# Kernel tuning notes

Hardware: AMD Instinct MI355X
Metric: run time of the kernel (lower is better)

The kernel has to match this reference:

```python
import jax, jax.numpy as jnp
import numpy as np

N, E, D, H, ED, L, G = 20000, 320000, 256, 256, 64, 4, 64


def setup_inputs() -> dict:
    key = jax.random.key(0)
    ks = jax.random.split(key, 24)
    w = lambda k, shape: jax.random.normal(k, shape, dtype=jnp.float32) * 0.05
    inp = {
        "x": jax.random.normal(ks[0], (N, D), dtype=jnp.float32),
        "edge_attr": jax.random.normal(ks[1], (E, ED), dtype=jnp.float32),
        "pos": jax.random.normal(ks[2], (N, 3), dtype=jnp.float32),
        "edge_index": jax.random.randint(ks[3], (2, E), 0, N, dtype=jnp.int32),
        "batch": jnp.sort(jax.random.randint(ks[4], (N,), 0, G, dtype=jnp.int32)),
        # stacked per-layer params [L, ...]
        "node_w": w(ks[5], (L, D, H)), "node_b": w(ks[6], (L, H)),
        "edge_w": w(ks[7], (L, ED, H)), "edge_b": w(ks[8], (L, H)),
        "msg_w1": w(ks[9], (L, 2 * H + 1, H)), "msg_b1": w(ks[10], (L, H)),
        "msg_w2": w(ks[11], (L, H, H)), "msg_b2": w(ks[12], (L, H)),
        "upd_w1": w(ks[13], (L, H, H)), "upd_b1": w(ks[14], (L, H)),
        "upd_w2": w(ks[15], (L, H, D)), "upd_b2": w(ks[16], (L, D)),
        # global pooling head
        "fc_w1": w(ks[17], (D, H)), "fc_b1": w(ks[18], (H,)),
        "fc_w2": w(ks[19], (H, 1)), "fc_b2": w(ks[20], (1,)),
    }
    return inp


def reference(x, edge_attr, pos, edge_index, batch,
              node_w, node_b, edge_w, edge_b,
              msg_w1, msg_b1, msg_w2, msg_b2,
              upd_w1, upd_b1, upd_w2, upd_b2,
              fc_w1, fc_b1, fc_w2, fc_b2):
    src = edge_index[0]  # x_j (source / message sender)
    dst = edge_index[1]  # x_i (target / aggregation index)
    # edge distance depends only on fixed pos/edge_index: compute once
    edge_dist = jnp.linalg.norm(pos[src] - pos[dst], axis=1, keepdims=True)  # [E,1]
    silu = jax.nn.silu
    for l in range(L):
        x_emb = x @ node_w[l] + node_b[l]                    # [N,H]
        e_emb = edge_attr @ edge_w[l] + edge_b[l]            # [E,H]
        m_in = jnp.concatenate([x_emb[dst], x_emb[src], edge_dist], axis=-1)  # [E,2H+1]
        m = silu(m_in @ msg_w1[l] + msg_b1[l])
        m = silu(m @ msg_w2[l] + msg_b2[l]) + e_emb          # [E,H]
        aggr = jax.ops.segment_sum(m, dst, num_segments=N)   # scatter-add into target nodes
        x = silu(aggr @ upd_w1[l] + upd_b1[l]) @ upd_w2[l] + upd_b2[l]  # [N,D]
    pooled = jax.ops.segment_sum(x, batch, num_segments=G)   # [G,D]
    out = silu(pooled @ fc_w1 + fc_b1) @ fc_w2 + fc_b2       # [G,1]
    return out
```

## Files before the change

kernel.cpp:

```cpp
#include <hip/hip_runtime.h>
#include <hip/hip_bf16.h>
#include <math.h>

#define N_NODES 20000
#define N_EDGES 320000
#define NGRAPH 64

typedef __attribute__((ext_vector_type(8))) short short8;
typedef __attribute__((ext_vector_type(4))) short short4x;
typedef __attribute__((ext_vector_type(4))) float f32x4;
typedef __attribute__((ext_vector_type(4))) unsigned uint4v;
typedef __attribute__((ext_vector_type(2))) unsigned uint2v;

__device__ __forceinline__ float silu_f(float v){ return v / (1.0f + __expf(-v)); }
__device__ __forceinline__ float bf2f(short s){
  unsigned u = ((unsigned)(unsigned short)s) << 16;
  float f; __builtin_memcpy(&f, &u, 4); return f;
}
__device__ __forceinline__ short f2bf(float f){
  unsigned u; __builtin_memcpy(&u, &f, 4);
  unsigned r = (u + 0x7FFFu + ((u >> 16) & 1u)) >> 16;
  return (short)r;
}
__device__ __forceinline__ unsigned pkcvt(float lo, float hi){
  unsigned r;
  asm("v_cvt_pk_bf16_f32 %0, %1, %2" : "=v"(r) : "v"(lo), "v"(hi));
  return r;
}
__device__ __forceinline__ float bf_lo(unsigned w){
  unsigned u = w << 16; float f; __builtin_memcpy(&f, &u, 4); return f;
}
__device__ __forceinline__ float bf_hi(unsigned w){
  unsigned u = w & 0xFFFF0000u; float f; __builtin_memcpy(&f, &u, 4); return f;
}

__global__ void k_hist(const int* __restrict__ ei, int* __restrict__ cnt){
  int e = blockIdx.x*256 + threadIdx.x;
  if (e >= N_EDGES) return;
  atomicAdd(&cnt[ei[N_EDGES + e]], 1);
}

__global__ void k_scan(const int* __restrict__ cnt, int* __restrict__ row_ptr,
                       int* __restrict__ off){
  __shared__ int ssum[256];
  int t = threadIdx.x;
  const int CHK = (N_NODES + 255)/256;
  int base = t*CHK;
  int s = 0;
  for(int i=0;i<CHK;i++){ int idx=base+i; if(idx<N_NODES) s += cnt[idx]; }
  ssum[t]=s; __syncthreads();
  for(int o=1;o<256;o<<=1){
    int v = (t>=o)? ssum[t-o] : 0;
    __syncthreads();
    ssum[t] += v;
    __syncthreads();
  }
  int pre = (t==0)? 0 : ssum[t-1];
  for(int i=0;i<CHK;i++){
    int idx=base+i; if(idx>=N_NODES) break;
    row_ptr[idx]=pre; off[idx]=pre; pre += cnt[idx];
  }
  if(t==255) row_ptr[N_NODES]=pre;
}

__global__ void k_scatter(const int* __restrict__ ei, int* __restrict__ off,
                          int* __restrict__ src_s, int* __restrict__ dst_s,
                          int* __restrict__ eid_s){
  int e = blockIdx.x*256 + threadIdx.x;
  if (e >= N_EDGES) return;
  int d = ei[N_EDGES + e];
  int p = atomicAdd(&off[d], 1);
  dst_s[p]=d; src_s[p]=ei[e]; eid_s[p]=e;
}

__global__ void k_dist_s(const int* __restrict__ src_s, const int* __restrict__ dst_s,
                         const float* __restrict__ pos, float* __restrict__ dist_s){
  int i = blockIdx.x*256 + threadIdx.x;
  if (i >= N_EDGES) return;
  int s = src_s[i], d = dst_s[i];
  float dx = pos[s*3+0]-pos[d*3+0];
  float dy = pos[s*3+1]-pos[d*3+1];
  float dz = pos[s*3+2]-pos[d*3+2];
  dist_s[i] = sqrtf(dx*dx+dy*dy+dz*dz);
}

__global__ void k_eaagg_s(const int* __restrict__ row_ptr, const int* __restrict__ eid_s,
                          const float* __restrict__ edge_attr, float* __restrict__ EA){
  int sub = threadIdx.x>>6, j = threadIdx.x&63;
  int d = blockIdx.x*4 + sub;
  if (d >= N_NODES) return;
  int b = row_ptr[d], e = row_ptr[d+1];
  float s = 0.f;
  for(int i=b;i<e;i++) s += edge_attr[(size_t)eid_s[i]*64 + j];
  EA[(size_t)d*96 + j] = s;
  if (j < 32) EA[(size_t)d*96 + 64 + j] = (j==0) ? (float)(e-b) : 0.f;
}

__global__ void k_f2b(const float* __restrict__ S, short* __restrict__ D, int n4){
  int i = blockIdx.x*256 + threadIdx.x;
  if (i >= n4) return;
  float4 v = ((const float4*)S)[i];
  uint2v o;
  o[0] = pkcvt(v.x, v.y);
  o[1] = pkcvt(v.z, v.w);
  *(uint2v*)&D[i*4] = o;
}

__global__ void k_transW(const float* __restrict__ msg_w1, const float* __restrict__ msg_w2,
                         const float* __restrict__ upd_w1, const float* __restrict__ upd_w2,
                         short* __restrict__ wT){
  int z = blockIdx.z; int l = z/5, w = z%5;
  const float* S;
  switch(w){
    case 0: S = msg_w1 + (size_t)l*513*256; break;
    case 1: S = msg_w1 + (size_t)l*513*256 + 256*256; break;
    case 2: S = msg_w2 + (size_t)l*256*256; break;
    case 3: S = upd_w1 + (size_t)l*256*256; break;
    default: S = upd_w2 + (size_t)l*256*256; break;
  }
  short* D = wT + (size_t)z*65536;
  __shared__ float t[32][33];
  int bx = blockIdx.x*32, by = blockIdx.y*32;
  int lx = threadIdx.x & 31, ly = threadIdx.x >> 5;
  #pragma unroll
  for(int r=0;r<4;r++){ int k = ly + r*8; t[k][lx] = S[(size_t)(by+k)*256 + bx+lx]; }
  __syncthreads();
  #pragma unroll
  for(int r=0;r<4;r++){
    int n = ly + r*8;
    D[(size_t)(bx+n)*256 + by+lx] = f2bf(t[lx][n]);
  }
}

__global__ void k_uw1ext(const short* __restrict__ wT, const float* __restrict__ edge_w,
                         const float* __restrict__ edge_b, short* __restrict__ uw1ext4){
  int n = blockIdx.x, l = blockIdx.y, tid = threadIdx.x;
  const short* uw1T = wT + (size_t)(l*5+3)*65536;
  short* dst = uw1ext4 + (size_t)l*256*352 + (size_t)n*352;
  dst[tid] = uw1T[(size_t)n*256 + tid];
  if (tid < 96){
    int c = tid;
    float s = 0.f;
    if (c < 64){
      const float* er = edge_w + (size_t)l*64*256 + (size_t)c*256;
      for(int m=0;m<256;m++) s += bf2f(uw1T[(size_t)n*256+m])*er[m];
    } else if (c == 64){
      const float* er = edge_b + (size_t)l*256;
      for(int m=0;m<256;m++) s += bf2f(uw1T[(size_t)n*256+m])*er[m];
    }
    dst[256 + c] = f2bf(s);
  }
}

__global__ void k_biasm_acc(const float* __restrict__ node_b, const float* __restrict__ msg_w1,
                            const float* __restrict__ msg_b1, float* __restrict__ biasm4){
  int j = threadIdx.x;
  int b = blockIdx.x, l = blockIdx.y;
  const float* nb  = node_b + l*256;
  const float* w1  = msg_w1 + (size_t)l*513*256;
  float* biasm = biasm4 + l*256;
  if (b == 16){ atomicAdd(&biasm[j], msg_b1[l*256+j]); return; }
  float s = 0.f;
  for(int k = b*16; k < b*16+16; k++)
    s += nb[k]*(w1[(size_t)k*256+j] + w1[(size_t)(256+k)*256+j]);
  atomicAdd(&biasm[j], s);
}

__global__ void k_biasfold(const float* __restrict__ upd_b2, const short* __restrict__ WabT4,
                           float* __restrict__ biasm4){
  int l = blockIdx.x + 1;
  int j = threadIdx.x;
  const float* ub2 = upd_b2 + (size_t)(l-1)*256;
  const short* W = WabT4 + (size_t)l*131072;
  float s = 0.f;
  for(int k=0;k<256;k++)
    s += ub2[k]*(bf2f(W[(size_t)j*256+k]) + bf2f(W[(size_t)(256+j)*256+k]));
  biasm4[l*256 + j] += s;
}

template<int K_REAL, int K_LDS, int OBF16>
__global__ __launch_bounds__(256)
void k_gemm_mfma(const short* __restrict__ A, const short* __restrict__ BT,
                 short* __restrict__ Cb, int M, int Nld,
                 int AzStr, int BzStr, int CzStr){
  __shared__ __align__(16) short As[32][K_LDS];
  const int CHL = K_LDS/8, CH = K_REAL/8;
  int tid = threadIdx.x;
  int zz = blockIdx.z;
  const short* Ab = A + (size_t)zz*AzStr;
  BT += (size_t)zz*BzStr;
  int m0 = blockIdx.y*32, n0 = blockIdx.x*256;
  for(int c = tid; c < 32*CHL; c += 256){
    int row = c / CHL, ch = c % CHL;
    uint4v v = (uint4v){0u,0u,0u,0u};
    if (ch < CH) v = *(const uint4v*)&Ab[(size_t)(m0+row)*K_REAL + ch*8];
    *(uint4v*)&As[row][(ch ^ (row&7))*8] = v;
  }
  __syncthreads();
  int wid = tid>>6, lane = tid&63, l15 = lane&15, lq = lane>>4;
  int ncol0 = n0 + wid*64;
  f32x4 acc[2][4];
  #pragma unroll
  for(int mt=0;mt<2;mt++)
    #pragma unroll
    for(int nt=0;nt<4;nt++) acc[mt][nt] = (f32x4){0.f,0.f,0.f,0.f};
  for(int k0=0;k0<K_REAL;k0+=32){
    int kc = k0 + 8*lq;
    short8 a[2], b[4];
    #pragma unroll
    for(int mt=0;mt<2;mt++){
      int row = mt*16 + l15;
      a[mt] = *(const short8*)&As[row][kc ^ ((row&7)<<3)];
    }
    #pragma unroll
    for(int nt=0;nt<4;nt++){
      int col = ncol0 + nt*16 + l15;
      b[nt] = *(const short8*)&BT[(size_t)col*K_REAL + kc];
    }
    #pragma unroll
    for(int mt=0;mt<2;mt++)
      #pragma unroll
      for(int nt=0;nt<4;nt++)
        acc[mt][nt] = __builtin_amdgcn_mfma_f32_16x16x32_bf16(a[mt], b[nt], acc[mt][nt], 0, 0, 0);
  }
  #pragma unroll
  for(int mt=0;mt<2;mt++){
    #pragma unroll
    for(int nt=0;nt<4;nt++){
      int col = ncol0 + nt*16 + l15;
      unsigned w01 = pkcvt(acc[mt][nt][0], acc[mt][nt][1]);
      unsigned w23 = pkcvt(acc[mt][nt][2], acc[mt][nt][3]);
      size_t base = (size_t)zz*CzStr + (size_t)(m0 + mt*16 + lq*4)*Nld + col;
      Cb[base]          = (short)(w01 & 0xFFFF);
      Cb[base +   Nld]  = (short)(w01>>16);
      Cb[base + 2*Nld]  = (short)(w23 & 0xFFFF);
      Cb[base + 3*Nld]  = (short)(w23>>16);
    }
  }
}

template<int K_REAL, int K_LDS, int AF32, int AEXT, int BIAS, int ACT, int OF32, int OBF16>
__global__ __launch_bounds__(256)
void k_gemm64(const void* __restrict__ A, const float* __restrict__ A2,
              const short* __restrict__ BT,
              const float* __restrict__ bias, float* __restrict__ Cf,
              short* __restrict__ Cb, int M, int Nld){
  __shared__ __align__(16) short As[64][K_LDS];
  const int CHL = K_LDS/8, CH = K_REAL/8;
  int tid = threadIdx.x;
  const short* Ab = (const short*)A;
  const float* Af = (const float*)A;
  int m0 = blockIdx.y*64, n0 = blockIdx.x*256;
  for(int c = tid; c < 64*CHL; c += 256){
    int row = c / CHL, ch = c % CHL;
    uint4v v = (uint4v){0u,0u,0u,0u};
    int grow = m0 + row;
    if (grow < M){
      if (AEXT){
        if (ch < 32){
          float4 f0 = *(const float4*)&Af[(size_t)grow*256 + ch*8];
          float4 f1 = *(const float4*)&Af[(size_t)grow*256 + ch*8 + 4];
          v[0]=pkcvt(f0.x,f0.y); v[1]=pkcvt(f0.z,f0.w); v[2]=pkcvt(f1.x,f1.y); v[3]=pkcvt(f1.z,f1.w);
        } else if (ch < 44){
          float4 f0 = *(const float4*)&A2[(size_t)grow*96 + (ch-32)*8];
          float4 f1 = *(const float4*)&A2[(size_t)grow*96 + (ch-32)*8 + 4];
          v[0]=pkcvt(f0.x,f0.y); v[1]=pkcvt(f0.z,f0.w); v[2]=pkcvt(f1.x,f1.y); v[3]=pkcvt(f1.z,f1.w);
        }
      } else if (ch < CH) {
        if (AF32){
          float4 f0 = *(const float4*)&Af[(size_t)grow*K_REAL + ch*8];
          float4 f1 = *(const float4*)&Af[(size_t)grow*K_REAL + ch*8 + 4];
          v[0]=pkcvt(f0.x,f0.y); v[1]=pkcvt(f0.z,f0.w); v[2]=pkcvt(f1.x,f1.y); v[3]=pkcvt(f1.z,f1.w);
        } else {
          v = *(const uint4v*)&Ab[(size_t)grow*K_REAL + ch*8];
        }
      }
    }
    *(uint4v*)&As[row][(ch ^ (row&7))*8] = v;
  }
  __syncthreads();
  int wid = tid>>6, lane = tid&63, l15 = lane&15, lq = lane>>4;
  int ncol0 = n0 + wid*64;
  f32x4 acc[4][4];
  #pragma unroll
  for(int mt=0;mt<4;mt++)
    #pragma unroll
    for(int nt=0;nt<4;nt++) acc[mt][nt] = (f32x4){0.f,0.f,0.f,0.f};
  for(int k0=0;k0<K_REAL;k0+=32){
    int kc = k0 + 8*lq;
    short8 a[4], b[4];
    #pragma unroll
    for(int mt=0;mt<4;mt++){
      int row = mt*16 + l15;
      a[mt] = *(const short8*)&As[row][kc ^ ((row&7)<<3)];
    }
    #pragma unroll
    for(int nt=0;nt<4;nt++){
      int col = ncol0 + nt*16 + l15;
      b[nt] = *(const short8*)&BT[(size_t)col*K_REAL + kc];
    }
    #pragma unroll
    for(int mt=0;mt<4;mt++)
      #pragma unroll
      for(int nt=0;nt<4;nt++)
        acc[mt][nt] = __builtin_amdgcn_mfma_f32_16x16x32_bf16(a[mt], b[nt], acc[mt][nt], 0, 0, 0);
  }
  #pragma unroll
  for(int mt=0;mt<4;mt++){
    int row0 = m0 + mt*16 + lq*4;
    if (row0 >= M) continue;
    #pragma unroll
    for(int nt=0;nt<4;nt++){
      int col = ncol0 + nt*16 + l15;
      float bb = BIAS ? bias[col] : 0.f;
      float vv[4];
      #pragma unroll
      for(int r=0;r<4;r++){
        float v = acc[mt][nt][r] + bb;
        if (ACT) v = silu_f(v);
        vv[r] = v;
      }
      if (OF32){
        #pragma unroll
        for(int r=0;r<4;r++)
          if (row0 + r < M)
            Cf[(size_t)(row0+r)*Nld + col] = vv[r];
      }
      if (OBF16){
        unsigned w01 = pkcvt(vv[0], vv[1]);
        unsigned w23 = pkcvt(vv[2], vv[3]);
        short ss[4] = {(short)(w01&0xFFFF),(short)(w01>>16),(short)(w23&0xFFFF),(short)(w23>>16)};
        #pragma unroll
        for(int r=0;r<4;r++)
          if (row0 + r < M)
            Cb[(size_t)(row0+r)*Nld + col] = ss[r];
      }
    }
  }
}

__global__ __launch_bounds__(256)
void k_edge_mfma(const short* __restrict__ t_ab,
                 const float* __restrict__ dist_s,
                 const int* __restrict__ src_s, const int* __restrict__ dst_s,
                 const float* __restrict__ w1c, const float* __restrict__ biasm,
                 const short* __restrict__ w2T, const float* __restrict__ b2,
                 float* __restrict__ aggr)
{
  __shared__ __align__(16) unsigned char ulds[256*34*2];
  short (*h)[256] = (short(*)[256])ulds;
  short* outl = (short*)ulds;
  __shared__ int sdst[32], ssrc[32];
  __shared__ float sdist[32];
  int tid = threadIdx.x;
  int e0 = blockIdx.x*32;
  if (tid < 32){
    sdst[tid] = dst_s[e0 + tid];
    ssrc[tid] = src_s[e0 + tid];
    sdist[tid] = dist_s[e0 + tid];
  }
  __syncthreads();
  int wid = tid>>6, lane = tid&63;
  int half = lane>>5, cl = lane&31;
  float wc8[8], bm8[8];
  {
    float4 w0 = *(const float4*)&w1c[8*cl], w1v = *(const float4*)&w1c[8*cl+4];
    float4 b0 = *(const float4*)&biasm[8*cl], b1v = *(const float4*)&biasm[8*cl+4];
    wc8[0]=w0.x; wc8[1]=w0.y; wc8[2]=w0.z; wc8[3]=w0.w;
    wc8[4]=w1v.x; wc8[5]=w1v.y; wc8[6]=w1v.z; wc8[7]=w1v.w;
    bm8[0]=b0.x; bm8[1]=b0.y; bm8[2]=b0.z; bm8[3]=b0.w;
    bm8[4]=b1v.x; bm8[5]=b1v.y; bm8[6]=b1v.z; bm8[7]=b1v.w;
  }
  #pragma unroll
  for(int p=0;p<4;p++){
    int e = wid*8 + p*2 + half;
    int d = sdst[e], s = ssrc[e];
    float de = sdist[e];
    short8 va = *(const short8*)&t_ab[(size_t)d*512 + 8*cl];
    short8 vb = *(const short8*)&t_ab[(size_t)s*512 + 256 + 8*cl];
    float f[8];
    #pragma unroll
    for(int i=0;i<8;i++)
      f[i] = silu_f(bf2f(va[i]) + bf2f(vb[i]) + de*wc8[i] + bm8[i]);
    uint4v hv;
    hv[0]=pkcvt(f[0],f[1]); hv[1]=pkcvt(f[2],f[3]); hv[2]=pkcvt(f[4],f[5]); hv[3]=pkcvt(f[6],f[7]);
    *(uint4v*)&h[e][(8*cl) ^ ((e&7)<<3)] = hv;
  }
  __syncthreads();

  int l15 = lane & 15, lq = lane >> 4;
  int nb = wid*64;
  f32x4 acc[2][4];
  #pragma unroll
  for(int mt=0;mt<2;mt++)
    #pragma unroll
    for(int nt=0;nt<4;nt++) acc[mt][nt] = (f32x4){0.f,0.f,0.f,0.f};

  for(int k0=0;k0<256;k0+=32){
    int kc = k0 + 8*lq;
    short8 a[2], b[4];
    #pragma unroll
    for(int mt=0;mt<2;mt++){
      int row = mt*16 + l15;
      a[mt] = *(const short8*)&h[row][kc ^ ((row&7)<<3)];
    }
    #pragma unroll
    for(int nt=0;nt<4;nt++){
      int col = nb + nt*16 + l15;
      b[nt] = *(const short8*)&w2T[(size_t)col*256 + kc];
    }
    #pragma unroll
    for(int mt=0;mt<2;mt++)
      #pragma unroll
      for(int nt=0;nt<4;nt++)
        acc[mt][nt] = __builtin_amdgcn_mfma_f32_16x16x32_bf16(a[mt], b[nt], acc[mt][nt], 0, 0, 0);
  }
  __syncthreads();

  #pragma unroll
  for(int mt=0;mt<2;mt++){
    #pragma unroll
    for(int nt=0;nt<4;nt++){
      int col = nb + nt*16 + l15;
      float bb = b2[col];
      float s0 = silu_f(acc[mt][nt][0] + bb);
      float s1 = silu_f(acc[mt][nt][1] + bb);
      float s2 = silu_f(acc[mt][nt][2] + bb);
      float s3 = silu_f(acc[mt][nt][3] + bb);
      unsigned* d32 = (unsigned*)&outl[col*34 + mt*16 + lq*4];
      d32[0] = pkcvt(s0, s1);
      d32[1] = pkcvt(s2, s3);
    }
  }
  __syncthreads();

  int j = tid;
  float accu = 0.f;
  int prev = sdst[0];
  #pragma unroll
  for(int e2=0;e2<32;e2+=2){
    unsigned w = *(const unsigned*)&outl[j*34 + e2];
    int d0 = sdst[e2], d1 = sdst[e2+1];
    if (d0 != prev){
      atomicAdd(&aggr[(size_t)prev*256 + j], accu);
      accu = 0.f; prev = d0;
    }
    accu += bf_lo(w);
    if (d1 != prev){
      atomicAdd(&aggr[(size_t)prev*256 + j], accu);
      accu = 0.f; prev = d1;
    }
    accu += bf_hi(w);
  }
  atomicAdd(&aggr[(size_t)prev*256 + j], accu);
}

__global__ void k_ghist(const int* __restrict__ batch, int* __restrict__ gcnt){
  int n = blockIdx.x*256 + threadIdx.x;
  if (n >= N_NODES) return;
  atomicAdd(&gcnt[batch[n]], 1);
}
__global__ void k_gscan(const int* __restrict__ gcnt, int* __restrict__ gptr){
  if (threadIdx.x == 0){
    int s = 0;
    for(int g=0; g<NGRAPH; g++){ gptr[g]=s; s += gcnt[g]; }
    gptr[NGRAPH] = s;
  }
}
__global__ void k_pool_seg(const float* __restrict__ x, const int* __restrict__ gptr,
                           float* __restrict__ pooled){
  int g = blockIdx.x, j = threadIdx.x;
  int b = gptr[g], e = gptr[g+1];
  float s = 0.f;
  for(int n=b; n<e; n++) s += x[(size_t)n*256 + j];
  pooled[g*256 + j] = s;
}

__global__ void k_head(const float* __restrict__ pooled, const float* __restrict__ fw1,
                       const float* __restrict__ fb1, const float* __restrict__ fw2,
                       const float* __restrict__ fb2, float* __restrict__ out){
  __shared__ float red[256];
  int g = blockIdx.x, j = threadIdx.x;
  float s = fb1[j];
  const float* p = &pooled[g*256];
  for(int k=0;k<256;k++) s += p[k]*fw1[k*256+j];
  float hv = silu_f(s)*fw2[j];
  red[j]=hv; __syncthreads();
  for(int off=128;off>0;off>>=1){ if(j<off) red[j]+=red[j+off]; __syncthreads(); }
  if(j==0) out[g] = red[0] + fb2[0];
}

extern "C" void kernel_launch(void* const* d_in, const int* in_sizes, int n_in,
                              void* d_out, int out_size, void* d_ws, size_t ws_size,
                              hipStream_t stream) {
  const float* x_in      = (const float*)d_in[0];
  const float* edge_attr = (const float*)d_in[1];
  const float* pos       = (const float*)d_in[2];
  const int*   ei        = (const int*)d_in[3];
  const int*   batch     = (const int*)d_in[4];
  const float* node_w    = (const float*)d_in[5];
  const float* node_b    = (const float*)d_in[6];
  const float* edge_w    = (const float*)d_in[7];
  const float* edge_b    = (const float*)d_in[8];
  const float* msg_w1    = (const float*)d_in[9];
  const float* msg_b1    = (const float*)d_in[10];
  const float* msg_w2    = (const float*)d_in[11];
  const float* msg_b2    = (const float*)d_in[12];
  const float* upd_w1    = (const float*)d_in[13];
  const float* upd_b1    = (const float*)d_in[14];
  const float* upd_w2    = (const float*)d_in[15];
  const float* upd_b2    = (const float*)d_in[16];
  const float* fc_w1     = (const float*)d_in[17];
  const float* fc_b1     = (const float*)d_in[18];
  const float* fc_w2     = (const float*)d_in[19];
  const float* fc_b2     = (const float*)d_in[20];
  float* out = (float*)d_out;

  float* ws = (float*)d_ws;
  int* cnt     = (int*)ws; ws += N_NODES;
  int* off     = (int*)ws; ws += N_NODES;
  int* row_ptr = (int*)ws; ws += N_NODES+4;
  int* src_s   = (int*)ws; ws += N_EDGES;
  int* dst_s   = (int*)ws; ws += N_EDGES;
  int* eid_s   = (int*)ws; ws += N_EDGES;
  float* dist_s= ws; ws += N_EDGES;
  int* gcnt    = (int*)ws; ws += NGRAPH;
  int* gptr    = (int*)ws; ws += NGRAPH+4;
  short* wT      = (short*)ws; ws += 20*65536/2;
  short* nw_bf4  = (short*)ws; ws += 4*65536/2;
  short* uw2_bf4 = (short*)ws; ws += 4*65536/2;
  short* uw1ext4 = (short*)ws; ws += 4*256*352/2 + 64;
  short* WabT4   = (short*)ws; ws += 4*131072/2;
  short* WfoldT4 = (short*)ws; ws += 3*131072/2;
  float* biasm4  = ws; ws += 4*256;
  short* h_bf   = (short*)ws; ws += (size_t)N_NODES*256/2;
  float* EA_aug = ws; ws += (size_t)N_NODES*96;
  float* tabreg = ws; ws += (size_t)N_NODES*256;
  float* aggr   = ws; ws += (size_t)N_NODES*256;
  float* pooled = ws; ws += NGRAPH*256;

  short* t_ab   = (short*)tabreg;
  float* xfinal = aggr;

  hipMemsetAsync(cnt, 0, N_NODES*sizeof(int), stream);
  k_hist<<<(N_EDGES+255)/256, 256, 0, stream>>>(ei, cnt);
  k_scan<<<1, 256, 0, stream>>>(cnt, row_ptr, off);
  k_scatter<<<(N_EDGES+255)/256, 256, 0, stream>>>(ei, off, src_s, dst_s, eid_s);
  k_dist_s<<<(N_EDGES+255)/256, 256, 0, stream>>>(src_s, dst_s, pos, dist_s);
  k_eaagg_s<<<N_NODES/4, 256, 0, stream>>>(row_ptr, eid_s, edge_attr, EA_aug);
  hipMemsetAsync(gcnt, 0, NGRAPH*sizeof(int), stream);
  k_ghist<<<(N_NODES+255)/256, 256, 0, stream>>>(batch, gcnt);
  k_gscan<<<1, 64, 0, stream>>>(gcnt, gptr);

  k_transW<<<dim3(8,8,20), 256, 0, stream>>>(msg_w1, msg_w2, upd_w1, upd_w2, wT);
  k_f2b<<<256, 256, 0, stream>>>(node_w, nw_bf4, 4*65536/4);
  k_f2b<<<256, 256, 0, stream>>>(upd_w2, uw2_bf4, 4*65536/4);
  k_uw1ext<<<dim3(256,4), 256, 0, stream>>>(wT, edge_w, edge_b, uw1ext4);
  hipMemsetAsync(biasm4, 0, 4*256*sizeof(float), stream);
  k_biasm_acc<<<dim3(17,4), 256, 0, stream>>>(node_b, msg_w1, msg_b1, biasm4);
  k_gemm_mfma<256,256,1><<<dim3(1,8,4), 256, 0, stream>>>(
      wT,         nw_bf4, WabT4,         256, 256, 5*65536, 65536, 131072);
  k_gemm_mfma<256,256,1><<<dim3(1,8,4), 256, 0, stream>>>(
      wT + 65536, nw_bf4, WabT4 + 65536, 256, 256, 5*65536, 65536, 131072);
  k_gemm_mfma<256,256,1><<<dim3(1,16,3), 256, 0, stream>>>(
      WabT4 + 131072, uw2_bf4, WfoldT4, 512, 256, 131072, 65536, 131072);
  k_biasfold<<<3, 256, 0, stream>>>(upd_b2, WabT4, biasm4);

  k_gemm64<256,256,1,0,0,0,0,1><<<dim3(2,313), 256, 0, stream>>>(
      x_in, nullptr, WabT4, nullptr, nullptr, t_ab, N_NODES, 512);

  for(int l=0;l<4;l++){
    const float* w1  = msg_w1 + (size_t)l*513*256;
    const float* mb2 = msg_b2 + l*256;
    const float* ub1 = upd_b1 + l*256;
    const float* ub2 = upd_b2 + l*256;
    const short* w2T_l  = wT + (size_t)(l*5+2)*65536;
    const short* uw2T_l = wT + (size_t)(l*5+4)*65536;

    hipMemsetAsync(aggr, 0, (size_t)N_NODES*256*sizeof(float), stream);

    k_edge_mfma<<<N_EDGES/32, 256, 0, stream>>>(t_ab, dist_s, src_s, dst_s,
                                                w1 + 512*256, biasm4 + l*256,
                                                w2T_l, mb2, aggr);

    k_gemm64<352,384,1,1,1,1,0,1><<<dim3(1,313), 256, 0, stream>>>(
        aggr, EA_aug, uw1ext4 + (size_t)l*256*352, ub1, nullptr, h_bf, N_NODES, 256);

    if (l < 3)
      k_gemm64<256,256,0,0,0,0,0,1><<<dim3(2,313), 256, 0, stream>>>(
          h_bf, nullptr, WfoldT4 + (size_t)l*131072, nullptr, nullptr, t_ab, N_NODES, 512);
    else
      k_gemm64<256,256,0,0,1,0,1,0><<<dim3(1,313), 256, 0, stream>>>(
          h_bf, nullptr, uw2T_l, ub2, xfinal, nullptr, N_NODES, 256);
  }

  k_pool_seg<<<NGRAPH, 256, 0, stream>>>(xfinal, gptr, pooled);
  k_head<<<NGRAPH, 256, 0, stream>>>(pooled, fc_w1, fc_b1, fc_w2, fc_b2, out);
}
```

Measured before the change: 1.271 ms.

## Fuse update MLP first layer with folded next-layer projection GEMM

For layers 0-2, adds a kernel that computes silu(aggr·W1+b1) for a 64-row tile, keeps the bf16 hidden activations in shared memory, and multiplies them by the folded next-layer weight to write t_ab directly. This removes a launch and the global write/read of the h_bf intermediate. In exchange, each block now does both GEMMs over 512 output columns with one 64-row tile per block (313 blocks). That can lower parallelism and occupancy because the kernel uses a large 48KB LDS footprint.

```diff
diff --git a/kernel.cpp b/kernel.cpp
--- a/kernel.cpp
+++ b/kernel.cpp
@@ -340,6 +340,124 @@
 }
 
 __global__ __launch_bounds__(256)
+void k_updfold(const float* __restrict__ aggr, const float* __restrict__ EA,
+               const short* __restrict__ uw1ext, const float* __restrict__ ub1,
+               const short* __restrict__ WfoldT, short* __restrict__ t_ab, int M)
+{
+  __shared__ __align__(16) short lds[64*384];
+  short (*As)[384] = (short(*)[384])lds;
+  short (*hh)[256] = (short(*)[256])lds;
+  int tid = threadIdx.x;
+  int m0 = blockIdx.y*64;
+  for(int c = tid; c < 64*48; c += 256){
+    int row = c / 48, ch = c % 48;
+    uint4v v = (uint4v){0u,0u,0u,0u};
+    int grow = m0 + row;
+    if (grow < M){
+      if (ch < 32){
+        float4 f0 = *(const float4*)&aggr[(size_t)grow*256 + ch*8];
+        float4 f1 = *(const float4*)&aggr[(size_t)grow*256 + ch*8 + 4];
+        v[0]=pkcvt(f0.x,f0.y); v[1]=pkcvt(f0.z,f0.w); v[2]=pkcvt(f1.x,f1.y); v[3]=pkcvt(f1.z,f1.w);
+      } else if (ch < 44){
+        float4 f0 = *(const float4*)&EA[(size_t)grow*96 + (ch-32)*8];
+        float4 f1 = *(const float4*)&EA[(size_t)grow*96 + (ch-32)*8 + 4];
+        v[0]=pkcvt(f0.x,f0.y); v[1]=pkcvt(f0.z,f0.w); v[2]=pkcvt(f1.x,f1.y); v[3]=pkcvt(f1.z,f1.w);
+      }
+    }
+    *(uint4v*)&As[row][(ch ^ (row&7))*8] = v;
+  }
+  __syncthreads();
+  int wid = tid>>6, lane = tid&63, l15 = lane&15, lq = lane>>4;
+  int ncol1 = wid*64;
+  f32x4 acc1[4][4];
+  #pragma unroll
+  for(int mt=0;mt<4;mt++)
+    #pragma unroll
+    for(int nt=0;nt<4;nt++) acc1[mt][nt] = (f32x4){0.f,0.f,0.f,0.f};
+  for(int k0=0;k0<352;k0+=32){
+    int kc = k0 + 8*lq;
+    short8 a[4], b[4];
+    #pragma unroll
+    for(int mt=0;mt<4;mt++){
+      int row = mt*16 + l15;
+      a[mt] = *(const short8*)&As[row][kc ^ ((row&7)<<3)];
+    }
+    #pragma unroll
+    for(int nt=0;nt<4;nt++){
+      int col = ncol1 + nt*16 + l15;
+      b[nt] = *(const short8*)&uw1ext[(size_t)col*352 + kc];
+    }
+    #pragma unroll
+    for(int mt=0;mt<4;mt++)
+      #pragma unroll
+      for(int nt=0;nt<4;nt++)
+        acc1[mt][nt] = __builtin_amdgcn_mfma_f32_16x16x32_bf16(a[mt], b[nt], acc1[mt][nt], 0, 0, 0);
+  }
+  __syncthreads();
+  #pragma unroll
+  for(int mt=0;mt<4;mt++){
+    #pragma unroll
+    for(int nt=0;nt<4;nt++){
+      int col = ncol1 + nt*16 + l15;
+      float bb = ub1[col];
+      unsigned w01 = pkcvt(silu_f(acc1[mt][nt][0] + bb), silu_f(acc1[mt][nt][1] + bb));
+      unsigned w23 = pkcvt(silu_f(acc1[mt][nt][2] + bb), silu_f(acc1[mt][nt][3] + bb));
+      short ss[4] = {(short)(w01&0xFFFF),(short)(w01>>16),(short)(w23&0xFFFF),(short)(w23>>16)};
+      #pragma unroll
+      for(int r=0;r<4;r++){
+        int row = mt*16 + lq*4 + r;
+        hh[row][((col>>3) ^ (row&7))*8 + (col&7)] = ss[r];
+      }
+    }
+  }
+  __syncthreads();
+  #pragma unroll
+  for(int hf=0; hf<2; hf++){
+    int ncol2 = wid*128 + hf*64;
+    f32x4 acc2[4][4];
+    #pragma unroll
+    for(int mt=0;mt<4;mt++)
+      #pragma unroll
+      for(int nt=0;nt<4;nt++) acc2[mt][nt] = (f32x4){0.f,0.f,0.f,0.f};
+    for(int k0=0;k0<256;k0+=32){
+      int kc = k0 + 8*lq;
+      short8 a[4], b[4];
+      #pragma unroll
+      for(int mt=0;mt<4;mt++){
+        int row = mt*16 + l15;
+        a[mt] = *(const short8*)&hh[row][kc ^ ((row&7)<<3)];
+      }
+      #pragma unroll
+      for(int nt=0;nt<4;nt++){
+        int col = ncol2 + nt*16 + l15;
+        b[nt] = *(const short8*)&WfoldT[(size_t)col*256 + kc];
+      }
+      #pragma unroll
+      for(int mt=0;mt<4;mt++)
+        #pragma unroll
+        for(int nt=0;nt<4;nt++)
+          acc2[mt][nt] = __builtin_amdgcn_mfma_f32_16x16x32_bf16(a[mt], b[nt], acc2[mt][nt], 0, 0, 0);
+    }
+    #pragma unroll
+    for(int mt=0;mt<4;mt++){
+      int row0 = m0 + mt*16 + lq*4;
+      if (row0 >= M) continue;
+      #pragma unroll
+      for(int nt=0;nt<4;nt++){
+        int col = ncol2 + nt*16 + l15;
+        unsigned w01 = pkcvt(acc2[mt][nt][0], acc2[mt][nt][1]);
+        unsigned w23 = pkcvt(acc2[mt][nt][2], acc2[mt][nt][3]);
+        short ss[4] = {(short)(w01&0xFFFF),(short)(w01>>16),(short)(w23&0xFFFF),(short)(w23>>16)};
+        #pragma unroll
+        for(int r=0;r<4;r++)
+          if (row0 + r < M)
+            t_ab[(size_t)(row0+r)*512 + col] = ss[r];
+      }
+    }
+  }
+}
+
+__global__ __launch_bounds__(256)
 void k_edge_mfma(const short* __restrict__ t_ab,
                  const float* __restrict__ dist_s,
                  const int* __restrict__ src_s, const int* __restrict__ dst_s,
@@ -583,15 +701,16 @@
                                                 w1 + 512*256, biasm4 + l*256,
                                                 w2T_l, mb2, aggr);
 
-    k_gemm64<352,384,1,1,1,1,0,1><<<dim3(1,313), 256, 0, stream>>>(
-        aggr, EA_aug, uw1ext4 + (size_t)l*256*352, ub1, nullptr, h_bf, N_NODES, 256);
-
-    if (l < 3)
-      k_gemm64<256,256,0,0,0,0,0,1><<<dim3(2,313), 256, 0, stream>>>(
-          h_bf, nullptr, WfoldT4 + (size_t)l*131072, nullptr, nullptr, t_ab, N_NODES, 512);
-    else
+    if (l < 3){
+      k_updfold<<<dim3(1,313), 256, 0, stream>>>(
+          aggr, EA_aug, uw1ext4 + (size_t)l*256*352, ub1,
+          WfoldT4 + (size_t)l*131072, t_ab, N_NODES);
+    } else {
+      k_gemm64<352,384,1,1,1,1,0,1><<<dim3(1,313), 256, 0, stream>>>(
+          aggr, EA_aug, uw1ext4 + (size_t)l*256*352, ub1, nullptr, h_bf, N_NODES, 256);
       k_gemm64<256,256,0,0,1,0,1,0><<<dim3(1,313), 256, 0, stream>>>(
           h_bf, nullptr, uw2T_l, ub2, xfinal, nullptr, N_NODES, 256);
+    }
   }
 
   k_pool_seg<<<NGRAPH, 256, 0, stream>>>(xfinal, gptr, pooled);
```

After: 1.267 ms. Within noise of the previous version (-0.3%).
